# Kernel tuning notes

Measured on AMD Instinct MI355X. Metric: run time of the kernel, lower is better.

Reference implementation:

```python
import jax, jax.numpy as jnp
import numpy as np

TOPK = 2  # config.topk_exp


def setup_inputs() -> dict:
    key = jax.random.key(0)
    ks = jax.random.split(key, 4)
    B, S, D, F, E = 4, 1024, 768, 3072, 8
    scale_in = 1.0 / np.sqrt(D)
    scale_hid = 1.0 / np.sqrt(F)
    return {
        "x": jax.random.normal(ks[0], (B, S, D), dtype=jnp.float32),
        "router_w": jax.random.normal(ks[1], (E, D), dtype=jnp.float32) * scale_in,
        "w_fc": jax.random.normal(ks[2], (E, D, F), dtype=jnp.float32) * scale_in,
        "b_fc": jnp.zeros((E, F), dtype=jnp.float32),
        "w_proj": jax.random.normal(ks[3], (E, F, D), dtype=jnp.float32) * scale_hid,
        "b_proj": jnp.zeros((E, D), dtype=jnp.float32),
    }


def _moe_forward(x, router_w, w_fc, b_fc, w_proj, b_proj):
    B, S, D = x.shape
    E = router_w.shape[0]
    xt = x.reshape(-1, D)  # [T, D] tokens
    # per-token router: Linear(D, E, bias=False)
    gate_logits = xt @ router_w.T  # [T, E]
    # topk_exp > 1: raw logits -> topk -> softmax over the k selected logits
    weights, selected = jax.lax.top_k(gate_logits, TOPK)  # [T, k]
    weights = jax.nn.softmax(weights.astype(jnp.float32), axis=1).astype(x.dtype)
    # combine weights per expert: w[t, e] = sum_k weights[t,k] * (selected[t,k]==e)
    onehot = jax.nn.one_hot(selected, E, dtype=x.dtype)  # [T, k, E]
    comb = jnp.einsum('tk,tke->te', weights, onehot)  # [T, E]
    # expert MLP (GPT-2 style: fc -> gelu -> proj), evaluated densely then combined
    h = jax.nn.gelu(jnp.einsum('td,edf->etf', xt, w_fc) + b_fc[:, None, :], approximate=False)
    y = jnp.einsum('etf,efd->etd', h, w_proj) + b_proj[:, None, :]  # [E, T, D]
    out = jnp.einsum('te,etd->td', comb, y)  # weighted scatter-combine
    return out.reshape(B, S, D)


def reference(x, router_w, w_fc, b_fc, w_proj, b_proj):
    return _moe_forward(x, router_w, w_fc, b_fc, w_proj, b_proj)
```

## Files before the change

### kernel.cpp

```cpp
#include <hip/hip_runtime.h>
#include <hip/hip_bf16.h>

#define TT 4096
#define DD 768
#define FF 3072
#define EE 8
#define NSLOT 8192
#define NSLOT_PAD 8320

#define WAITCNT_VM4 0x0F74
#define WAITCNT_VM3 0x0F73

typedef __attribute__((ext_vector_type(8))) short bf16x8;
typedef __attribute__((ext_vector_type(4))) float f32x4;
typedef const __attribute__((address_space(1))) void* gas1_t;
typedef __attribute__((address_space(3))) void* las3_t;

__global__ __launch_bounds__(256) void router2_kernel(const float* __restrict__ x,
    const float* __restrict__ rw, int* __restrict__ tokE, float* __restrict__ tokW,
    int* __restrict__ blkCnt) {
  __shared__ float rws[EE * 832];
  __shared__ int cnt_s[EE];
  int tid = threadIdx.x;
  if (tid < EE) cnt_s[tid] = 0;
#pragma unroll
  for (int k = 0; k < 6; ++k) {
    int c = tid + k * 256;
    int e = c / 192, rem = c % 192;
    int s = rem / 12, i = rem % 12;
    float4 v = *(const float4*)&rw[e * DD + s * 48 + i * 4];
    *(float4*)&rws[e * 832 + s * 52 + i * 4] = v;
  }
  __syncthreads();
  int lane = tid & 63;
  int sl = lane & 15;
  int t = blockIdx.x * 16 + (tid >> 6) * 4 + (lane >> 4);
  const float4* xp = (const float4*)(x + (size_t)t * DD + sl * 48);
  float acc[EE];
#pragma unroll
  for (int e = 0; e < EE; ++e) acc[e] = 0.f;
#pragma unroll
  for (int i = 0; i < 12; ++i) {
    float4 xv = xp[i];
#pragma unroll
    for (int e = 0; e < EE; ++e) {
      float4 rv = *(const float4*)&rws[e * 832 + sl * 52 + i * 4];
      acc[e] = fmaf(xv.x, rv.x, fmaf(xv.y, rv.y, fmaf(xv.z, rv.z, fmaf(xv.w, rv.w, acc[e]))));
    }
  }
#pragma unroll
  for (int off = 8; off > 0; off >>= 1) {
#pragma unroll
    for (int e = 0; e < EE; ++e) acc[e] += __shfl_xor(acc[e], off);
  }
  if (sl == 0) {
    float v0 = -1e30f; int e0 = 0;
#pragma unroll
    for (int e = 0; e < EE; ++e) { if (acc[e] > v0) { v0 = acc[e]; e0 = e; } }
    float v1 = -1e30f; int e1 = 0;
#pragma unroll
    for (int e = 0; e < EE; ++e) { if (e != e0 && acc[e] > v1) { v1 = acc[e]; e1 = e; } }
    float w1 = 1.f / (1.f + __expf(v0 - v1));
    float w0 = 1.f - w1;
    tokE[2 * t] = e0; tokE[2 * t + 1] = e1;
    tokW[2 * t] = w0; tokW[2 * t + 1] = w1;
    atomicAdd(&cnt_s[e0], 1);
    atomicAdd(&cnt_s[e1], 1);
  }
  __syncthreads();
  if (tid < EE) blkCnt[blockIdx.x * EE + tid] = cnt_s[tid];
}

__global__ __launch_bounds__(256) void offsets2_kernel(const int* __restrict__ blkCnt,
    int* __restrict__ offs, int* __restrict__ blkBase,
    int* __restrict__ tile1, int* __restrict__ tile2, int* __restrict__ meta) {
  __shared__ int wsum[4][EE];
  int tid = threadIdx.x;
  int lane = tid & 63, w = tid >> 6;
  int c[EE], s[EE];
#pragma unroll
  for (int e = 0; e < EE; ++e) { c[e] = blkCnt[tid * EE + e]; s[e] = c[e]; }
#pragma unroll
  for (int off = 1; off < 64; off <<= 1) {
#pragma unroll
    for (int e = 0; e < EE; ++e) {
      int v = __shfl_up(s[e], off);
      if (lane >= off) s[e] += v;
    }
  }
  if (lane == 63) {
#pragma unroll
    for (int e = 0; e < EE; ++e) wsum[w][e] = s[e];
  }
  __syncthreads();
#pragma unroll
  for (int e = 0; e < EE; ++e) {
    int pre = 0;
    for (int w2 = 0; w2 < w; ++w2) pre += wsum[w2][e];
    s[e] += pre;
  }
  int tot[EE];
#pragma unroll
  for (int e = 0; e < EE; ++e) tot[e] = wsum[0][e] + wsum[1][e] + wsum[2][e] + wsum[3][e];
  int offl[EE + 1];
  offl[0] = 0;
#pragma unroll
  for (int e = 0; e < EE; ++e) offl[e + 1] = offl[e] + tot[e];
#pragma unroll
  for (int e = 0; e < EE; ++e) blkBase[tid * EE + e] = offl[e] + s[e] - c[e];
  if (tid == 0) {
    for (int e = 0; e <= EE; ++e) offs[e] = offl[e];
    int n1 = 0, n2 = 0;
    for (int e = 0; e < EE; ++e) { n1 += (tot[e] + 127) / 128; n2 += (tot[e] + 63) / 64; }
    meta[0] = n1; meta[1] = n2;
  }
  if (tid < EE) {
    int p1 = 0, p2 = 0;
    for (int e = 0; e < tid; ++e) { p1 += (tot[e] + 127) / 128; p2 += (tot[e] + 63) / 64; }
    for (int m = 0; m < tot[tid]; m += 128) tile1[p1++] = (tid << 20) | m;
    for (int m = 0; m < tot[tid]; m += 64)  tile2[p2++] = (tid << 20) | m;
  }
}

__global__ __launch_bounds__(256) void scatter_gather2_kernel(const float* __restrict__ x,
    const int* __restrict__ tokE, const float* __restrict__ tokW,
    const int* __restrict__ blkBase, int* __restrict__ slotIdx, float* __restrict__ slotW,
    __hip_bfloat16* __restrict__ Xg) {
  __shared__ int base_s[EE], lcur[EE];
  __shared__ int sl_s[16][2];
  int tid = threadIdx.x;
  int b = blockIdx.x;
  if (tid < EE) { base_s[tid] = blkBase[b * EE + tid]; lcur[tid] = 0; }
  __syncthreads();
  if (tid < 16) {
    int t = b * 16 + tid;
    int e0 = tokE[2 * t], e1 = tokE[2 * t + 1];
    int s0 = base_s[e0] + atomicAdd(&lcur[e0], 1);
    int s1 = base_s[e1] + atomicAdd(&lcur[e1], 1);
    slotIdx[2 * t] = s0; slotIdx[2 * t + 1] = s1;
    slotW[s0] = tokW[2 * t]; slotW[s1] = tokW[2 * t + 1];
    sl_s[tid][0] = s0; sl_s[tid][1] = s1;
  }
  __syncthreads();
  int k = tid >> 4, p = tid & 15;
  int t = b * 16 + k;
  int s0 = sl_s[k][0], s1 = sl_s[k][1];
  const float4* src = (const float4*)(x + (size_t)t * DD + p * 48);
  ushort4* d0 = (ushort4*)(Xg + (size_t)s0 * DD + p * 48);
  ushort4* d1 = (ushort4*)(Xg + (size_t)s1 * DD + p * 48);
#pragma unroll
  for (int i = 0; i < 12; ++i) {
    float4 v = src[i];
    union { ushort4 u; __hip_bfloat16 h[4]; } cv;
    cv.h[0] = __float2bfloat16(v.x);
    cv.h[1] = __float2bfloat16(v.y);
    cv.h[2] = __float2bfloat16(v.z);
    cv.h[3] = __float2bfloat16(v.w);
    d0[i] = cv.u;
    d1[i] = cv.u;
  }
}

__global__ void transpose_convert_kernel(const float* __restrict__ w_fc, __hip_bfloat16* __restrict__ wfcT,
                                         const float* __restrict__ w_proj, __hip_bfloat16* __restrict__ wprojT) {
  __shared__ float tile[64][65];
  int bx = blockIdx.x;
  const float* S; __hip_bfloat16* D; int K, N, n0, k0;
  if (bx < 576) { S = w_fc;   D = wfcT;   K = DD; N = FF; n0 = (bx % 48) * 64; k0 = (bx / 48) * 64; }
  else { bx -= 576; S = w_proj; D = wprojT; K = FF; N = DD; n0 = (bx % 12) * 64; k0 = (bx / 12) * 64; }
  S += (size_t)blockIdx.z * K * N;
  D += (size_t)blockIdx.z * K * N;
  int tid = threadIdx.x;
#pragma unroll
  for (int i = 0; i < 4; ++i) {
    int slot = i * 256 + tid;
    int r = slot >> 4, c4 = slot & 15;
    float4 v = *(const float4*)&S[(size_t)(k0 + r) * N + n0 + c4 * 4];
    tile[r][c4 * 4 + 0] = v.x; tile[r][c4 * 4 + 1] = v.y;
    tile[r][c4 * 4 + 2] = v.z; tile[r][c4 * 4 + 3] = v.w;
  }
  __syncthreads();
#pragma unroll
  for (int i = 0; i < 4; ++i) {
    int slot = i * 256 + tid;
    int n = slot >> 4, kc = slot & 15;
    union { ushort4 u; __hip_bfloat16 h[4]; } cv;
    cv.h[0] = __float2bfloat16(tile[kc * 4 + 0][n]);
    cv.h[1] = __float2bfloat16(tile[kc * 4 + 1][n]);
    cv.h[2] = __float2bfloat16(tile[kc * 4 + 2][n]);
    cv.h[3] = __float2bfloat16(tile[kc * 4 + 3][n]);
    *(ushort4*)&D[(size_t)(n0 + n) * K + k0 + kc * 4] = cv.u;
  }
}

__device__ __forceinline__ float gelu_f(float v) {
  float z = v * 0.70710678118654752f;
  float az = fabsf(z);
  float t = 1.0f / (1.0f + 0.3275911f * az);
  float poly = t * (0.254829592f + t * (-0.284496736f + t * (1.421413741f +
               t * (-1.453152027f + t * 1.061405429f))));
  float erf_abs = 1.0f - poly * __expf(-az * az);
  float erf = copysignf(erf_abs, z);
  return 0.5f * v * (1.0f + erf);
}

__device__ __forceinline__ int swz4(int m) { return (m + (m >> 2)) & 3; }

__global__ __launch_bounds__(256) void gemm1_kernel(const __hip_bfloat16* __restrict__ Xg,
    const __hip_bfloat16* __restrict__ wfcT, const float* __restrict__ b_fc,
    __hip_bfloat16* __restrict__ H, const int* __restrict__ offs,
    const int* __restrict__ tile1, const int* __restrict__ meta) {
  __shared__ __align__(16) short As[2][128 * 32];
  __shared__ __align__(16) short Bs[2][128 * 32];
  if ((int)blockIdx.y >= meta[0]) return;
  int tv = tile1[blockIdx.y];
  int e = tv >> 20;
  int m_base = tv & 0xFFFFF;
  int off_e = offs[e];
  int n_e = offs[e + 1] - off_e;
  int n0 = blockIdx.x * 128;
  const short* A = (const short*)Xg + (size_t)(off_e + m_base) * DD;
  const short* B = (const short*)wfcT + (size_t)e * FF * DD + (size_t)n0 * DD;
  int tid = threadIdx.x;
  int lane = tid & 63, wid = tid >> 6;
  int l15 = lane & 15, q = lane >> 4;
  int wm = wid & 1, wn = wid >> 1;
  int fs0 = tid, fs1 = tid + 256;
  int m0 = fs0 >> 2, c0 = (fs0 & 3) ^ swz4(m0);
  int m1 = fs1 >> 2, c1 = (fs1 & 3) ^ swz4(m1);
  const short* gA0 = A + (size_t)m0 * DD + c0 * 8;
  const short* gA1 = A + (size_t)m1 * DD + c1 * 8;
  const short* gB0 = B + (size_t)m0 * DD + c0 * 8;
  const short* gB1 = B + (size_t)m1 * DD + c1 * 8;
  int aoff[4], boff[4];
#pragma unroll
  for (int mi = 0; mi < 4; ++mi) {
    int r = wm * 64 + mi * 16 + l15;
    aoff[mi] = (r * 4 + (q ^ swz4(r))) * 8;
  }
#pragma unroll
  for (int ni = 0; ni < 4; ++ni) {
    int r = wn * 64 + ni * 16 + l15;
    boff[ni] = (r * 4 + (q ^ swz4(r))) * 8;
  }
  f32x4 acc[4][4] = {};
  __builtin_amdgcn_global_load_lds((gas1_t)gA0, (las3_t)(&As[0][0] + fs0 * 8), 16, 0, 0);
  __builtin_amdgcn_global_load_lds((gas1_t)gA1, (las3_t)(&As[0][0] + fs1 * 8), 16, 0, 0);
  __builtin_amdgcn_global_load_lds((gas1_t)gB0, (las3_t)(&Bs[0][0] + fs0 * 8), 16, 0, 0);
  __builtin_amdgcn_global_load_lds((gas1_t)gB1, (las3_t)(&Bs[0][0] + fs1 * 8), 16, 0, 0);
  gA0 += 32; gA1 += 32; gB0 += 32; gB1 += 32;
  for (int it = 0; it < DD / 32; ++it) {
    int cur = it & 1, nxt = cur ^ 1;
    short* curA = &As[cur][0];
    short* curB = &Bs[cur][0];
    __builtin_amdgcn_s_barrier();
    __builtin_amdgcn_global_load_lds((gas1_t)gA0, (las3_t)(&As[nxt][0] + fs0 * 8), 16, 0, 0);
    __builtin_amdgcn_global_load_lds((gas1_t)gA1, (las3_t)(&As[nxt][0] + fs1 * 8), 16, 0, 0);
    __builtin_amdgcn_global_load_lds((gas1_t)gB0, (las3_t)(&Bs[nxt][0] + fs0 * 8), 16, 0, 0);
    __builtin_amdgcn_global_load_lds((gas1_t)gB1, (las3_t)(&Bs[nxt][0] + fs1 * 8), 16, 0, 0);
    gA0 += 32; gA1 += 32; gB0 += 32; gB1 += 32;
    __builtin_amdgcn_s_waitcnt(WAITCNT_VM4);
    __builtin_amdgcn_s_barrier();
    bf16x8 af[4], bfr[4];
#pragma unroll
    for (int mi = 0; mi < 4; ++mi) af[mi] = *(const bf16x8*)(curA + aoff[mi]);
#pragma unroll
    for (int ni = 0; ni < 4; ++ni) bfr[ni] = *(const bf16x8*)(curB + boff[ni]);
#pragma unroll
    for (int mi = 0; mi < 4; ++mi)
#pragma unroll
      for (int ni = 0; ni < 4; ++ni)
        acc[mi][ni] = __builtin_amdgcn_mfma_f32_16x16x32_bf16(af[mi], bfr[ni], acc[mi][ni], 0, 0, 0);
  }
  float bias[4];
#pragma unroll
  for (int ni = 0; ni < 4; ++ni) bias[ni] = b_fc[e * FF + n0 + wn * 64 + ni * 16 + l15];
  __hip_bfloat16* Hp = H + (size_t)(off_e + m_base) * FF + n0;
#pragma unroll
  for (int mi = 0; mi < 4; ++mi) {
#pragma unroll
    for (int r = 0; r < 4; ++r) {
      int ml = wm * 64 + mi * 16 + q * 4 + r;
      if (m_base + ml < n_e) {
#pragma unroll
        for (int ni = 0; ni < 4; ++ni) {
          int nl = wn * 64 + ni * 16 + l15;
          float v = acc[mi][ni][r] + bias[ni];
          Hp[(size_t)ml * FF + nl] = __float2bfloat16(gelu_f(v));
        }
      }
    }
  }
}

__global__ __launch_bounds__(256) void gemm2_kernel(const __hip_bfloat16* __restrict__ H,
    const __hip_bfloat16* __restrict__ wprojT, const float* __restrict__ b_proj,
    const float* __restrict__ slotW, float* __restrict__ Yw, const int* __restrict__ offs,
    const int* __restrict__ tile2, const int* __restrict__ meta) {
  __shared__ __align__(16) short As[2][64 * 32];
  __shared__ __align__(16) short Bs[2][128 * 32];
  if ((int)blockIdx.y >= meta[1]) return;
  int tv = tile2[blockIdx.y];
  int e = tv >> 20;
  int m_base = tv & 0xFFFFF;
  int off_e = offs[e];
  int n_e = offs[e + 1] - off_e;
  int n0 = blockIdx.x * 128;
  const short* A = (const short*)H + (size_t)(off_e + m_base) * FF;
  const short* B = (const short*)wprojT + (size_t)e * DD * FF + (size_t)n0 * FF;
  int tid = threadIdx.x;
  int lane = tid & 63, wid = tid >> 6;
  int l15 = lane & 15, q = lane >> 4;
  int wm = wid & 1, wn = wid >> 1;
  int fs0 = tid, fs1 = tid + 256;
  int m0 = fs0 >> 2, c0 = (fs0 & 3) ^ swz4(m0);
  int m1 = fs1 >> 2, c1 = (fs1 & 3) ^ swz4(m1);
  const short* gA0 = A + (size_t)m0 * FF + c0 * 8;
  const short* gB0 = B + (size_t)m0 * FF + c0 * 8;
  const short* gB1 = B + (size_t)m1 * FF + c1 * 8;
  int aoff[2], boff[4];
#pragma unroll
  for (int mi = 0; mi < 2; ++mi) {
    int r = wm * 32 + mi * 16 + l15;
    aoff[mi] = (r * 4 + (q ^ swz4(r))) * 8;
  }
#pragma unroll
  for (int ni = 0; ni < 4; ++ni) {
    int r = wn * 64 + ni * 16 + l15;
    boff[ni] = (r * 4 + (q ^ swz4(r))) * 8;
  }
  f32x4 acc[2][4] = {};
  __builtin_amdgcn_global_load_lds((gas1_t)gA0, (las3_t)(&As[0][0] + fs0 * 8), 16, 0, 0);
  __builtin_amdgcn_global_load_lds((gas1_t)gB0, (las3_t)(&Bs[0][0] + fs0 * 8), 16, 0, 0);
  __builtin_amdgcn_global_load_lds((gas1_t)gB1, (las3_t)(&Bs[0][0] + fs1 * 8), 16, 0, 0);
  gA0 += 32; gB0 += 32; gB1 += 32;
  for (int it = 0; it < FF / 32; ++it) {
    int cur = it & 1, nxt = cur ^ 1;
    short* curA = &As[cur][0];
    short* curB = &Bs[cur][0];
    __builtin_amdgcn_s_barrier();
    __builtin_amdgcn_global_load_lds((gas1_t)gA0, (las3_t)(&As[nxt][0] + fs0 * 8), 16, 0, 0);
    __builtin_amdgcn_global_load_lds((gas1_t)gB0, (las3_t)(&Bs[nxt][0] + fs0 * 8), 16, 0, 0);
    __builtin_amdgcn_global_load_lds((gas1_t)gB1, (las3_t)(&Bs[nxt][0] + fs1 * 8), 16, 0, 0);
    gA0 += 32; gB0 += 32; gB1 += 32;
    __builtin_amdgcn_s_waitcnt(WAITCNT_VM3);
    __builtin_amdgcn_s_barrier();
    bf16x8 af[2], bfr[4];
#pragma unroll
    for (int mi = 0; mi < 2; ++mi) af[mi] = *(const bf16x8*)(curA + aoff[mi]);
#pragma unroll
    for (int ni = 0; ni < 4; ++ni) bfr[ni] = *(const bf16x8*)(curB + boff[ni]);
#pragma unroll
    for (int mi = 0; mi < 2; ++mi)
#pragma unroll
      for (int ni = 0; ni < 4; ++ni)
        acc[mi][ni] = __builtin_amdgcn_mfma_f32_16x16x32_bf16(af[mi], bfr[ni], acc[mi][ni], 0, 0, 0);
  }
  float bias[4];
#pragma unroll
  for (int ni = 0; ni < 4; ++ni) bias[ni] = b_proj[e * DD + n0 + wn * 64 + ni * 16 + l15];
  float* Yp = Yw + (size_t)(off_e + m_base) * DD + n0;
#pragma unroll
  for (int mi = 0; mi < 2; ++mi) {
#pragma unroll
    for (int r = 0; r < 4; ++r) {
      int ml = wm * 32 + mi * 16 + q * 4 + r;
      if (m_base + ml < n_e) {
        float w = slotW[off_e + m_base + ml];
#pragma unroll
        for (int ni = 0; ni < 4; ++ni) {
          int nl = wn * 64 + ni * 16 + l15;
          Yp[(size_t)ml * DD + nl] = w * (acc[mi][ni][r] + bias[ni]);
        }
      }
    }
  }
}

__global__ void combine_kernel(const float* __restrict__ Yw, const int* __restrict__ slotIdx,
                               float* __restrict__ out) {
  int idx = blockIdx.x * 256 + threadIdx.x;
  int t = idx / (DD / 4);
  int g = idx - t * (DD / 4);
  int s0 = slotIdx[2 * t], s1 = slotIdx[2 * t + 1];
  const float4 a = ((const float4*)(Yw + (size_t)s0 * DD))[g];
  const float4 b = ((const float4*)(Yw + (size_t)s1 * DD))[g];
  float4 o;
  o.x = a.x + b.x; o.y = a.y + b.y; o.z = a.z + b.z; o.w = a.w + b.w;
  ((float4*)(out + (size_t)t * DD))[g] = o;
}

extern "C" void kernel_launch(void* const* d_in, const int* in_sizes, int n_in,
                              void* d_out, int out_size, void* d_ws, size_t ws_size,
                              hipStream_t stream) {
  const float* x        = (const float*)d_in[0];
  const float* router_w = (const float*)d_in[1];
  const float* w_fc     = (const float*)d_in[2];
  const float* b_fc     = (const float*)d_in[3];
  const float* w_proj   = (const float*)d_in[4];
  const float* b_proj   = (const float*)d_in[5];
  float* out = (float*)d_out;

  char* p = (char*)d_ws;
  auto alloc = [&](size_t bytes) {
    char* r = p;
    p += (bytes + 255) & ~(size_t)255;
    return r;
  };
  __hip_bfloat16* wfcT   = (__hip_bfloat16*)alloc((size_t)EE * FF * DD * 2);
  __hip_bfloat16* wprojT = (__hip_bfloat16*)alloc((size_t)EE * DD * FF * 2);
  __hip_bfloat16* Xg     = (__hip_bfloat16*)alloc((size_t)NSLOT_PAD * DD * 2);
  __hip_bfloat16* H      = (__hip_bfloat16*)alloc((size_t)NSLOT_PAD * FF * 2);
  float*          Yw     = (float*)alloc((size_t)NSLOT_PAD * DD * 4);
  int*   tokE    = (int*)alloc(TT * 2 * 4);
  float* tokW    = (float*)alloc(TT * 2 * 4);
  int*   slotIdx = (int*)alloc(TT * 2 * 4);
  float* slotW   = (float*)alloc(NSLOT_PAD * 4);
  int*   blkCnt  = (int*)alloc(256 * EE * 4);
  int*   blkBase = (int*)alloc(256 * EE * 4);
  int*   tile1   = (int*)alloc(128 * 4);
  int*   tile2   = (int*)alloc(256 * 4);
  int*   offs    = (int*)alloc(64);
  int*   meta    = (int*)alloc(64);

  router2_kernel<<<256, 256, 0, stream>>>(x, router_w, tokE, tokW, blkCnt);
  offsets2_kernel<<<1, 256, 0, stream>>>(blkCnt, offs, blkBase, tile1, tile2, meta);
  scatter_gather2_kernel<<<256, 256, 0, stream>>>(x, tokE, tokW, blkBase, slotIdx, slotW, Xg);
  transpose_convert_kernel<<<dim3(1152, 1, EE), 256, 0, stream>>>(w_fc, wfcT, w_proj, wprojT);
  gemm1_kernel<<<dim3(FF / 128, 72), 256, 0, stream>>>(Xg, wfcT, b_fc, H, offs, tile1, meta);
  gemm2_kernel<<<dim3(DD / 128, 136), 256, 0, stream>>>(H, wprojT, b_proj, slotW, Yw, offs, tile2, meta);
  combine_kernel<<<TT * (DD / 4) / 256, 256, 0, stream>>>(Yw, slotIdx, out);
}
```

Before: 397.3 us.

## Fuse combine into gemm2 via atomic scatter-add and widen N tile

The separate combine kernel and the fp32 Yw intermediate buffer are removed. gemm2 now atomically adds its weighted rows straight into the zeroed output, using a new slot-to-token map. gemm2's N tile grows from 128 to 384, so the grid has 2 column blocks instead of 6, each warp owns a 64x96 sub-tile, and more LDS is used. The scatter_gather copy is also re-indexed so memory accesses coalesce. The costs are a memset, fp32 atomics with non-deterministic summation order, fewer blocks in flight and more register pressure.

Result: no change. 390.9 us (-1.6%).

```diff
diff --git a/kernel.cpp b/kernel.cpp
--- a/kernel.cpp
+++ b/kernel.cpp
@@ -9,7 +9,7 @@
 #define NSLOT_PAD 8320
 
 #define WAITCNT_VM4 0x0F74
-#define WAITCNT_VM3 0x0F73
+#define WAITCNT_VM7 0x0F77
 
 typedef __attribute__((ext_vector_type(8))) short bf16x8;
 typedef __attribute__((ext_vector_type(4))) float f32x4;
@@ -125,7 +125,7 @@
 __global__ __launch_bounds__(256) void scatter_gather2_kernel(const float* __restrict__ x,
     const int* __restrict__ tokE, const float* __restrict__ tokW,
     const int* __restrict__ blkBase, int* __restrict__ slotIdx, float* __restrict__ slotW,
-    __hip_bfloat16* __restrict__ Xg) {
+    int* __restrict__ slotTok, __hip_bfloat16* __restrict__ Xg) {
   __shared__ int base_s[EE], lcur[EE];
   __shared__ int sl_s[16][2];
   int tid = threadIdx.x;
@@ -139,25 +139,27 @@
     int s1 = base_s[e1] + atomicAdd(&lcur[e1], 1);
     slotIdx[2 * t] = s0; slotIdx[2 * t + 1] = s1;
     slotW[s0] = tokW[2 * t]; slotW[s1] = tokW[2 * t + 1];
+    slotTok[s0] = t; slotTok[s1] = t;
     sl_s[tid][0] = s0; sl_s[tid][1] = s1;
   }
   __syncthreads();
   int k = tid >> 4, p = tid & 15;
   int t = b * 16 + k;
   int s0 = sl_s[k][0], s1 = sl_s[k][1];
-  const float4* src = (const float4*)(x + (size_t)t * DD + p * 48);
-  ushort4* d0 = (ushort4*)(Xg + (size_t)s0 * DD + p * 48);
-  ushort4* d1 = (ushort4*)(Xg + (size_t)s1 * DD + p * 48);
+  const float4* src = (const float4*)(x + (size_t)t * DD);
+  ushort4* d0 = (ushort4*)(Xg + (size_t)s0 * DD);
+  ushort4* d1 = (ushort4*)(Xg + (size_t)s1 * DD);
 #pragma unroll
   for (int i = 0; i < 12; ++i) {
-    float4 v = src[i];
+    int idx = i * 16 + p;
+    float4 v = src[idx];
     union { ushort4 u; __hip_bfloat16 h[4]; } cv;
     cv.h[0] = __float2bfloat16(v.x);
     cv.h[1] = __float2bfloat16(v.y);
     cv.h[2] = __float2bfloat16(v.z);
     cv.h[3] = __float2bfloat16(v.w);
-    d0[i] = cv.u;
-    d1[i] = cv.u;
+    d0[idx] = cv.u;
+    d1[idx] = cv.u;
   }
 }
 
@@ -295,99 +297,97 @@
 
 __global__ __launch_bounds__(256) void gemm2_kernel(const __hip_bfloat16* __restrict__ H,
     const __hip_bfloat16* __restrict__ wprojT, const float* __restrict__ b_proj,
-    const float* __restrict__ slotW, float* __restrict__ Yw, const int* __restrict__ offs,
+    const float* __restrict__ slotW, const int* __restrict__ slotTok,
+    float* __restrict__ out, const int* __restrict__ offs,
     const int* __restrict__ tile2, const int* __restrict__ meta) {
   __shared__ __align__(16) short As[2][64 * 32];
-  __shared__ __align__(16) short Bs[2][128 * 32];
+  __shared__ __align__(16) short Bs[2][384 * 32];
   if ((int)blockIdx.y >= meta[1]) return;
   int tv = tile2[blockIdx.y];
   int e = tv >> 20;
   int m_base = tv & 0xFFFFF;
   int off_e = offs[e];
   int n_e = offs[e + 1] - off_e;
-  int n0 = blockIdx.x * 128;
+  int n0 = blockIdx.x * 384;
   const short* A = (const short*)H + (size_t)(off_e + m_base) * FF;
   const short* B = (const short*)wprojT + (size_t)e * DD * FF + (size_t)n0 * FF;
   int tid = threadIdx.x;
   int lane = tid & 63, wid = tid >> 6;
   int l15 = lane & 15, q = lane >> 4;
-  int wm = wid & 1, wn = wid >> 1;
-  int fs0 = tid, fs1 = tid + 256;
-  int m0 = fs0 >> 2, c0 = (fs0 & 3) ^ swz4(m0);
-  int m1 = fs1 >> 2, c1 = (fs1 & 3) ^ swz4(m1);
-  const short* gA0 = A + (size_t)m0 * FF + c0 * 8;
-  const short* gB0 = B + (size_t)m0 * FF + c0 * 8;
-  const short* gB1 = B + (size_t)m1 * FF + c1 * 8;
-  int aoff[2], boff[4];
-#pragma unroll
-  for (int mi = 0; mi < 2; ++mi) {
-    int r = wm * 32 + mi * 16 + l15;
+  int mA = tid >> 2, cA = (tid & 3) ^ swz4(mA);
+  const short* gA = A + (size_t)mA * FF + cA * 8;
+  const short* gB[6];
+  int fsB[6];
+#pragma unroll
+  for (int i = 0; i < 6; ++i) {
+    int fs = tid + i * 256;
+    int m = fs >> 2, c = (fs & 3) ^ swz4(m);
+    fsB[i] = fs;
+    gB[i] = B + (size_t)m * FF + c * 8;
+  }
+  int aoff[4], boff[6];
+#pragma unroll
+  for (int mi = 0; mi < 4; ++mi) {
+    int r = mi * 16 + l15;
     aoff[mi] = (r * 4 + (q ^ swz4(r))) * 8;
   }
 #pragma unroll
-  for (int ni = 0; ni < 4; ++ni) {
-    int r = wn * 64 + ni * 16 + l15;
+  for (int ni = 0; ni < 6; ++ni) {
+    int r = wid * 96 + ni * 16 + l15;
     boff[ni] = (r * 4 + (q ^ swz4(r))) * 8;
   }
-  f32x4 acc[2][4] = {};
-  __builtin_amdgcn_global_load_lds((gas1_t)gA0, (las3_t)(&As[0][0] + fs0 * 8), 16, 0, 0);
-  __builtin_amdgcn_global_load_lds((gas1_t)gB0, (las3_t)(&Bs[0][0] + fs0 * 8), 16, 0, 0);
-  __builtin_amdgcn_global_load_lds((gas1_t)gB1, (las3_t)(&Bs[0][0] + fs1 * 8), 16, 0, 0);
-  gA0 += 32; gB0 += 32; gB1 += 32;
+  f32x4 acc[4][6] = {};
+  __builtin_amdgcn_global_load_lds((gas1_t)gA, (las3_t)(&As[0][0] + tid * 8), 16, 0, 0);
+#pragma unroll
+  for (int i = 0; i < 6; ++i)
+    __builtin_amdgcn_global_load_lds((gas1_t)gB[i], (las3_t)(&Bs[0][0] + fsB[i] * 8), 16, 0, 0);
+  gA += 32;
+#pragma unroll
+  for (int i = 0; i < 6; ++i) gB[i] += 32;
   for (int it = 0; it < FF / 32; ++it) {
     int cur = it & 1, nxt = cur ^ 1;
     short* curA = &As[cur][0];
     short* curB = &Bs[cur][0];
     __builtin_amdgcn_s_barrier();
-    __builtin_amdgcn_global_load_lds((gas1_t)gA0, (las3_t)(&As[nxt][0] + fs0 * 8), 16, 0, 0);
-    __builtin_amdgcn_global_load_lds((gas1_t)gB0, (las3_t)(&Bs[nxt][0] + fs0 * 8), 16, 0, 0);
-    __builtin_amdgcn_global_load_lds((gas1_t)gB1, (las3_t)(&Bs[nxt][0] + fs1 * 8), 16, 0, 0);
-    gA0 += 32; gB0 += 32; gB1 += 32;
-    __builtin_amdgcn_s_waitcnt(WAITCNT_VM3);
+    __builtin_amdgcn_global_load_lds((gas1_t)gA, (las3_t)(&As[nxt][0] + tid * 8), 16, 0, 0);
+#pragma unroll
+    for (int i = 0; i < 6; ++i)
+      __builtin_amdgcn_global_load_lds((gas1_t)gB[i], (las3_t)(&Bs[nxt][0] + fsB[i] * 8), 16, 0, 0);
+    gA += 32;
+#pragma unroll
+    for (int i = 0; i < 6; ++i) gB[i] += 32;
+    __builtin_amdgcn_s_waitcnt(WAITCNT_VM7);
     __builtin_amdgcn_s_barrier();
-    bf16x8 af[2], bfr[4];
-#pragma unroll
-    for (int mi = 0; mi < 2; ++mi) af[mi] = *(const bf16x8*)(curA + aoff[mi]);
-#pragma unroll
-    for (int ni = 0; ni < 4; ++ni) bfr[ni] = *(const bf16x8*)(curB + boff[ni]);
-#pragma unroll
-    for (int mi = 0; mi < 2; ++mi)
-#pragma unroll
-      for (int ni = 0; ni < 4; ++ni)
+    bf16x8 af[4], bfr[6];
+#pragma unroll
+    for (int mi = 0; mi < 4; ++mi) af[mi] = *(const bf16x8*)(curA + aoff[mi]);
+#pragma unroll
+    for (int ni = 0; ni < 6; ++ni) bfr[ni] = *(const bf16x8*)(curB + boff[ni]);
+#pragma unroll
+    for (int mi = 0; mi < 4; ++mi)
+#pragma unroll
+      for (int ni = 0; ni < 6; ++ni)
         acc[mi][ni] = __builtin_amdgcn_mfma_f32_16x16x32_bf16(af[mi], bfr[ni], acc[mi][ni], 0, 0, 0);
   }
-  float bias[4];
-#pragma unroll
-  for (int ni = 0; ni < 4; ++ni) bias[ni] = b_proj[e * DD + n0 + wn * 64 + ni * 16 + l15];
-  float* Yp = Yw + (size_t)(off_e + m_base) * DD + n0;
-#pragma unroll
-  for (int mi = 0; mi < 2; ++mi) {
+  float bias[6];
+#pragma unroll
+  for (int ni = 0; ni < 6; ++ni) bias[ni] = b_proj[e * DD + n0 + wid * 96 + ni * 16 + l15];
+#pragma unroll
+  for (int mi = 0; mi < 4; ++mi) {
 #pragma unroll
     for (int r = 0; r < 4; ++r) {
-      int ml = wm * 32 + mi * 16 + q * 4 + r;
+      int ml = mi * 16 + q * 4 + r;
       if (m_base + ml < n_e) {
-        float w = slotW[off_e + m_base + ml];
-#pragma unroll
-        for (int ni = 0; ni < 4; ++ni) {
-          int nl = wn * 64 + ni * 16 + l15;
-          Yp[(size_t)ml * DD + nl] = w * (acc[mi][ni][r] + bias[ni]);
-        }
+        int slot = off_e + m_base + ml;
+        float w = slotW[slot];
+        int tok = slotTok[slot];
+        float* op = out + (size_t)tok * DD + n0 + wid * 96;
+#pragma unroll
+        for (int ni = 0; ni < 6; ++ni)
+          atomicAdd(&op[ni * 16 + l15], w * (acc[mi][ni][r] + bias[ni]));
       }
     }
   }
-}
-
-__global__ void combine_kernel(const float* __restrict__ Yw, const int* __restrict__ slotIdx,
-                               float* __restrict__ out) {
-  int idx = blockIdx.x * 256 + threadIdx.x;
-  int t = idx / (DD / 4);
-  int g = idx - t * (DD / 4);
-  int s0 = slotIdx[2 * t], s1 = slotIdx[2 * t + 1];
-  const float4 a = ((const float4*)(Yw + (size_t)s0 * DD))[g];
-  const float4 b = ((const float4*)(Yw + (size_t)s1 * DD))[g];
-  float4 o;
-  o.x = a.x + b.x; o.y = a.y + b.y; o.z = a.z + b.z; o.w = a.w + b.w;
-  ((float4*)(out + (size_t)t * DD))[g] = o;
 }
 
 extern "C" void kernel_launch(void* const* d_in, const int* in_sizes, int n_in,
@@ -411,11 +411,11 @@
   __hip_bfloat16* wprojT = (__hip_bfloat16*)alloc((size_t)EE * DD * FF * 2);
   __hip_bfloat16* Xg     = (__hip_bfloat16*)alloc((size_t)NSLOT_PAD * DD * 2);
   __hip_bfloat16* H      = (__hip_bfloat16*)alloc((size_t)NSLOT_PAD * FF * 2);
-  float*          Yw     = (float*)alloc((size_t)NSLOT_PAD * DD * 4);
   int*   tokE    = (int*)alloc(TT * 2 * 4);
   float* tokW    = (float*)alloc(TT * 2 * 4);
   int*   slotIdx = (int*)alloc(TT * 2 * 4);
   float* slotW   = (float*)alloc(NSLOT_PAD * 4);
+  int*   slotTok = (int*)alloc(NSLOT_PAD * 4);
   int*   blkCnt  = (int*)alloc(256 * EE * 4);
   int*   blkBase = (int*)alloc(256 * EE * 4);
   int*   tile1   = (int*)alloc(128 * 4);
@@ -423,11 +423,11 @@
   int*   offs    = (int*)alloc(64);
   int*   meta    = (int*)alloc(64);
 
+  hipMemsetAsync(out, 0, (size_t)out_size * 4, stream);
   router2_kernel<<<256, 256, 0, stream>>>(x, router_w, tokE, tokW, blkCnt);
   offsets2_kernel<<<1, 256, 0, stream>>>(blkCnt, offs, blkBase, tile1, tile2, meta);
-  scatter_gather2_kernel<<<256, 256, 0, stream>>>(x, tokE, tokW, blkBase, slotIdx, slotW, Xg);
+  scatter_gather2_kernel<<<256, 256, 0, stream>>>(x, tokE, tokW, blkBase, slotIdx, slotW, slotTok, Xg);
   transpose_convert_kernel<<<dim3(1152, 1, EE), 256, 0, stream>>>(w_fc, wfcT, w_proj, wprojT);
   gemm1_kernel<<<dim3(FF / 128, 72), 256, 0, stream>>>(Xg, wfcT, b_fc, H, offs, tile1, meta);
-  gemm2_kernel<<<dim3(DD / 128, 136), 256, 0, stream>>>(H, wprojT, b_proj, slotW, Yw, offs, tile2, meta);
-  combine_kernel<<<TT * (DD / 4) / 256, 256, 0, stream>>>(Yw, slotIdx, out);
-}
+  gemm2_kernel<<<dim3(DD / 384, 136), 256, 0, stream>>>(H, wprojT, b_proj, slotW, slotTok, out, offs, tile2, meta);
+}
```
